# Performance work log

Measured on AMD Instinct MI355X. Metric: run time of the kernel, lower is better.

Reference implementation:

```python
import jax, jax.numpy as jnp
import numpy as np

H = 16          # num_heads
LN_EPS = 1e-5


def _layernorm(x, g, b):
    mu = jnp.mean(x, axis=-1, keepdims=True)
    var = jnp.mean(jnp.square(x - mu), axis=-1, keepdims=True)
    return (x - mu) * jax.lax.rsqrt(var + LN_EPS) * g + b


def setup_inputs() -> dict:
    key = jax.random.key(0)
    ks = jax.random.split(key, 4)
    B, T, D = 32, 1024, 1024
    s = 1.0 / np.sqrt(D)
    return {
        "x": jax.random.normal(ks[0], (B, T, D), dtype=jnp.float32),
        "ln_g": jnp.ones((D,), jnp.float32),
        "ln_b": jnp.zeros((D,), jnp.float32),
        "Wq": jax.random.normal(ks[1], (D, D), dtype=jnp.float32) * s,
        "bq": jnp.zeros((D,), jnp.float32),
        "Wk": jax.random.normal(ks[2], (D, D), dtype=jnp.float32) * s,
        "bk": jnp.zeros((D,), jnp.float32),
        "Wv": jax.random.normal(ks[3], (D, D), dtype=jnp.float32) * s,
        "bv": jnp.zeros((D,), jnp.float32),
    }


def reference(x, ln_g, ln_b, Wq, bq, Wk, bk, Wv, bv):
    B, T, D = x.shape
    d = D // H
    xn = _layernorm(x, ln_g, ln_b)                       # [B,T,D]
    # torch Linear: y = x @ W.T + b, W is [out, in]
    q = jnp.einsum('btd,ed->bte', xn, Wq) + bq
    k = jnp.einsum('btd,ed->bte', xn, Wk) + bk
    v = (jnp.einsum('btd,ed->bte', xn, Wv) + bv).reshape(B, T, H, d)
    q = jax.nn.softmax(q.reshape(B, T, H, d), axis=-1)   # softmax over head dim
    k = jax.nn.softmax(k.reshape(B, T, H, d), axis=1)    # softmax over sequence
    # linear attention: context [B,H,d,d], then project queries through it
    attn = jnp.einsum('bnhd,bnhl->bhdl', k, v)
    y = jnp.einsum('bnhd,bhdl->bnhl', q, attn).reshape(B, T, D)
    return x + y
```

## Files before the change

### kernel.cpp

```cpp
#include <hip/hip_runtime.h>
#include <stdint.h>

typedef __attribute__((ext_vector_type(4))) float  f32x4;
typedef __attribute__((ext_vector_type(8))) short  short8;
typedef __attribute__((ext_vector_type(4))) short  short4v;
typedef __attribute__((ext_vector_type(2))) unsigned int uint2v;

#define DEV __device__ __forceinline__

DEV float b2f(unsigned short u) { return __uint_as_float(((unsigned)u) << 16); }
DEV unsigned short f2b(float f) {
  unsigned u = __float_as_uint(f);
  return (unsigned short)((u + 0x7fffu + ((u >> 16) & 1u)) >> 16);
}

#define AS1C(p) ((const __attribute__((address_space(1))) void*)(uintptr_t)(p))
#define AS3(p)  ((__attribute__((address_space(3))) void*)(unsigned)(uintptr_t)(p))
DEV void gload16(const void* g, void* l) {
  __builtin_amdgcn_global_load_lds(AS1C(g), AS3(l), 16, 0, 0);
}

static constexpr int B_ = 32, T_ = 1024, D_ = 1024;
static constexpr int M_ = B_ * T_;
static constexpr int N3 = 3 * D_;

__global__ __launch_bounds__(256) void prep_kernel(
    const float* __restrict__ Wq, const float* __restrict__ Wk, const float* __restrict__ Wv,
    const float* __restrict__ bq, const float* __restrict__ bk, const float* __restrict__ bv,
    const float* __restrict__ x, const float* __restrict__ lng, const float* __restrict__ lnb,
    unsigned short* __restrict__ Wcat, float* __restrict__ bias,
    float* __restrict__ ksum, unsigned short* __restrict__ xn)
{
  int bid = blockIdx.x;
  int tid = threadIdx.x;
  if (bid < 3072) {
    int idx = bid * 256 + tid;
    int which = idx >> 18;
    int rem   = idx & 262143;
    const float* src = which == 0 ? Wq : (which == 1 ? Wk : Wv);
    f32x4 v = reinterpret_cast<const f32x4*>(src)[rem];
    uint2v p;
    p[0] = (unsigned)f2b(v[0]) | ((unsigned)f2b(v[1]) << 16);
    p[1] = (unsigned)f2b(v[2]) | ((unsigned)f2b(v[3]) << 16);
    reinterpret_cast<uint2v*>(Wcat)[idx] = p;
    if (idx < 3072) {
      const float* bsrc = idx < 1024 ? bq : (idx < 2048 ? bk : bv);
      bias[idx] = bsrc[idx & 1023];
    }
    if (idx < 32768) ksum[idx] = 0.f;
    return;
  }
  int row = bid - 3072;
  const f32x4 v = reinterpret_cast<const f32x4*>(x + (size_t)row * D_)[tid];
  float s  = v[0] + v[1] + v[2] + v[3];
  float s2 = v[0]*v[0] + v[1]*v[1] + v[2]*v[2] + v[3]*v[3];
  #pragma unroll
  for (int o = 32; o > 0; o >>= 1) { s += __shfl_down(s, o); s2 += __shfl_down(s2, o); }
  __shared__ float rs_[4], rs2_[4];
  int lane = tid & 63, wave = tid >> 6;
  if (lane == 0) { rs_[wave] = s; rs2_[wave] = s2; }
  __syncthreads();
  float S  = rs_[0] + rs_[1] + rs_[2] + rs_[3];
  float S2 = rs2_[0] + rs2_[1] + rs2_[2] + rs2_[3];
  float mu = S * (1.f / D_);
  float var = S2 * (1.f / D_) - mu * mu;
  float rstd = rsqrtf(var + 1e-5f);
  const f32x4 gg = reinterpret_cast<const f32x4*>(lng)[tid];
  const f32x4 bb = reinterpret_cast<const f32x4*>(lnb)[tid];
  float y0 = (v[0]-mu)*rstd*gg[0] + bb[0];
  float y1 = (v[1]-mu)*rstd*gg[1] + bb[1];
  float y2 = (v[2]-mu)*rstd*gg[2] + bb[2];
  float y3 = (v[3]-mu)*rstd*gg[3] + bb[3];
  uint2v p;
  p[0] = (unsigned)f2b(y0) | ((unsigned)f2b(y1) << 16);
  p[1] = (unsigned)f2b(y2) | ((unsigned)f2b(y3) << 16);
  reinterpret_cast<uint2v*>(xn + (size_t)row * D_)[tid] = p;
}

__global__ __launch_bounds__(512, 2) void gemm_qkv(
    const unsigned short* __restrict__ A,
    const unsigned short* __restrict__ Bm,
    const float* __restrict__ bias,
    unsigned short* __restrict__ C,
    float* __restrict__ ksum)
{
  __shared__ alignas(16) short lds[4 * 16384];
  const int tid = threadIdx.x;
  constexpr int nbn = N3 / 256;
  constexpr int nwg = (M_ / 256) * nbn;
  int wg = blockIdx.x;
  int swzb = (wg & 7) * (nwg >> 3) + (wg >> 3);
  int bm = swzb / nbn, bn = swzb % nbn;
  int arow = bm * 256, bcol = bn * 256;
  int lane = tid & 63, wave = tid >> 6;
  int wr = wave >> 2, wc = wave & 3;
  int g = lane >> 4, r = lane & 15;

  const unsigned short* Ab = A  + (size_t)arow * 1024;
  const unsigned short* Bb = Bm + (size_t)bcol * 1024;

  int rho = (wave << 4) | (lane >> 2);
  int pg  = (lane & 3) ^ ((rho >> 1) & 3);
  size_t gR0 = (size_t)rho * 1024 + pg * 8;
  size_t gR1 = (size_t)(rho + 128) * 1024 + pg * 8;
  int lofs = wave * 512;

  #define STAGE_A(t) { short* bb0 = lds + (((t) & 3) << 14); int k2 = (t) << 5; \
    gload16(Ab + k2 + gR0, (void*)(bb0 + lofs)); \
    gload16(Ab + k2 + gR1, (void*)(bb0 + 4096 + lofs)); }
  #define STAGE_B(t) { short* bb0 = lds + (((t) & 3) << 14); int k2 = (t) << 5; \
    gload16(Bb + k2 + gR0, (void*)(bb0 + 8192 + lofs)); \
    gload16(Bb + k2 + gR1, (void*)(bb0 + 12288 + lofs)); }

  f32x4 acc[8][4] = {};
  STAGE_A(0); STAGE_B(0);
  STAGE_A(1); STAGE_B(1);
  STAGE_A(2); STAGE_B(2);
  asm volatile("s_waitcnt vmcnt(8)" ::: "memory");
  __builtin_amdgcn_s_barrier();

  for (int t = 0; t < 32; ++t) {
    const short* bufA = lds + ((t & 3) << 14);
    const short* bufB = bufA + 8192;
    short8 a[8], bfr[4];
    #pragma unroll
    for (int mi = 0; mi < 8; ++mi) {
      int row = wr * 128 + mi * 16 + r;
      a[mi] = *(const short8*)(bufA + row * 32 + ((g ^ ((row >> 1) & 3)) << 3));
    }
    #pragma unroll
    for (int ni = 0; ni < 4; ++ni) {
      int row = wc * 64 + ni * 16 + r;
      bfr[ni] = *(const short8*)(bufB + row * 32 + ((g ^ ((row >> 1) & 3)) << 3));
    }
    if (t < 29) { STAGE_A(t + 3); STAGE_B(t + 3); }
    __builtin_amdgcn_s_setprio(1);
    #pragma unroll
    for (int mi = 0; mi < 8; ++mi)
      #pragma unroll
      for (int ni = 0; ni < 4; ++ni)
        acc[mi][ni] = __builtin_amdgcn_mfma_f32_16x16x32_bf16(a[mi], bfr[ni], acc[mi][ni], 0, 0, 0);
    __builtin_amdgcn_s_setprio(0);
    if (t < 29)       { asm volatile("s_waitcnt vmcnt(8)" ::: "memory"); }
    else if (t == 29) { asm volatile("s_waitcnt vmcnt(4)" ::: "memory"); }
    else if (t == 30) { asm volatile("s_waitcnt vmcnt(0)" ::: "memory"); }
    __builtin_amdgcn_s_barrier();
  }
  #undef STAGE_A
  #undef STAGE_B

  float bs[4];
  #pragma unroll
  for (int ni = 0; ni < 4; ++ni) bs[ni] = bias[bcol + wc * 64 + ni * 16 + r];
  bool isK = (bcol >= 1024 && bcol < 2048);
  if (isK) {
    float ks[4] = {0.f, 0.f, 0.f, 0.f};
    #pragma unroll
    for (int mi = 0; mi < 8; ++mi)
      #pragma unroll
      for (int j = 0; j < 4; ++j) {
        int rowl = wr * 128 + mi * 16 + 4 * g + j;
        size_t rb = (size_t)(arow + rowl) * N3 + bcol + wc * 64 + r;
        #pragma unroll
        for (int ni = 0; ni < 4; ++ni) {
          unsigned short cv = f2b(acc[mi][ni][j] + bs[ni]);
          C[rb + ni * 16] = cv;
          ks[ni] += __expf(b2f(cv));
        }
      }
    int b = arow >> 10;
    #pragma unroll
    for (int ni = 0; ni < 4; ++ni) {
      float s = ks[ni];
      s += __shfl_xor(s, 16);
      s += __shfl_xor(s, 32);
      if (g == 0)
        atomicAdd(&ksum[b * 1024 + (bcol - 1024) + wc * 64 + ni * 16 + r], s);
    }
  } else {
    #pragma unroll
    for (int mi = 0; mi < 8; ++mi)
      #pragma unroll
      for (int j = 0; j < 4; ++j) {
        int rowl = wr * 128 + mi * 16 + 4 * g + j;
        size_t rb = (size_t)(arow + rowl) * N3 + bcol + wc * 64 + r;
        #pragma unroll
        for (int ni = 0; ni < 4; ++ni)
          C[rb + ni * 16] = f2b(acc[mi][ni][j] + bs[ni]);
      }
  }
}

__global__ __launch_bounds__(256) void attn_kernel(
    const unsigned short* __restrict__ qkv, const float* __restrict__ ksum,
    unsigned short* __restrict__ attnP)
{
  int bid = blockIdx.x;
  int bh = bid >> 2, tq = bid & 3;
  int b = bh >> 4, h = bh & 15;
  int tid = threadIdx.x;
  int cgrp = tid & 7, trow = tid >> 3;
  int lane = tid & 63, wave = tid >> 6;
  int g = lane >> 4, r = lane & 15;
  __shared__ alignas(16) short lK[64 * 40];
  __shared__ alignas(16) short lV[64 * 40];
  const unsigned short* kb = qkv + ((size_t)(b * T_ + tq * 256)) * N3 + D_     + h * 64;
  const unsigned short* vb = qkv + ((size_t)(b * T_ + tq * 256)) * N3 + 2 * D_ + h * 64;
  float inv[8];
  const float* kp = ksum + b * 1024 + h * 64 + cgrp * 8;
  #pragma unroll
  for (int j = 0; j < 8; ++j) inv[j] = 1.f / kp[j];
  f32x4 acc[4] = {};
  short8 kv = *(const short8*)(kb + (size_t)trow * N3 + cgrp * 8);
  short8 vv = *(const short8*)(vb + (size_t)trow * N3 + cgrp * 8);
  for (int tc = 0; tc < 8; ++tc) {
    __syncthreads();
    #pragma unroll
    for (int j = 0; j < 8; ++j) {
      lK[(cgrp * 8 + j) * 40 + trow] =
          (short)f2b(__expf(b2f((unsigned short)kv[j])) * inv[j]);
      lV[(cgrp * 8 + j) * 40 + trow] = vv[j];
    }
    __syncthreads();
    if (tc < 7) {
      kv = *(const short8*)(kb + (size_t)((tc + 1) * 32 + trow) * N3 + cgrp * 8);
      vv = *(const short8*)(vb + (size_t)((tc + 1) * 32 + trow) * N3 + cgrp * 8);
    }
    short8 af = *(const short8*)(lK + (16 * wave + r) * 40 + 8 * g);
    #pragma unroll
    for (int ni = 0; ni < 4; ++ni) {
      short8 bf = *(const short8*)(lV + (16 * ni + r) * 40 + 8 * g);
      acc[ni] = __builtin_amdgcn_mfma_f32_16x16x32_bf16(af, bf, acc[ni], 0, 0, 0);
    }
  }
  unsigned short* op = attnP + (size_t)bid * 4096;
  #pragma unroll
  for (int ni = 0; ni < 4; ++ni)
    #pragma unroll
    for (int j = 0; j < 4; ++j) {
      int m = 16 * wave + 4 * g + j;
      int n = 16 * ni + r;
      op[(size_t)n * 64 + m] = f2b(acc[ni][j]);
    }
}

__global__ __launch_bounds__(256) void attn_reduce(
    const unsigned short* __restrict__ attnP, unsigned short* __restrict__ attnT)
{
  int bh = blockIdx.x;
  int tid = threadIdx.x;
  const unsigned short* p0 = attnP + ((size_t)bh << 2) * 4096;
  unsigned short* o = attnT + (size_t)bh * 4096;
  #pragma unroll
  for (int it = 0; it < 2; ++it) {
    int i = (it * 256 + tid) * 8;
    short8 s0 = *(const short8*)(p0 + i);
    short8 s1 = *(const short8*)(p0 + 4096 + i);
    short8 s2 = *(const short8*)(p0 + 8192 + i);
    short8 s3 = *(const short8*)(p0 + 12288 + i);
    short8 ov;
    #pragma unroll
    for (int j = 0; j < 8; ++j) {
      float s = b2f((unsigned short)s0[j]) + b2f((unsigned short)s1[j])
              + b2f((unsigned short)s2[j]) + b2f((unsigned short)s3[j]);
      ov[j] = (short)f2b(s);
    }
    *(short8*)(o + i) = ov;
  }
}

__global__ __launch_bounds__(256) void out_kernel(
    const unsigned short* __restrict__ qkv, const unsigned short* __restrict__ attnT,
    const float* __restrict__ x, float* __restrict__ out)
{
  int bid = blockIdx.x;
  int bh = bid >> 3, mt = bid & 7;
  int b = bh >> 4, h = bh & 15;
  int tid = threadIdx.x;
  int lane = tid & 63, wave = tid >> 6;
  int g = lane >> 4, r = lane & 15;
  __shared__ alignas(16) short lAT[64 * 72];
  __shared__ float lO[128][66];
  int rr = tid >> 4, c4 = (tid & 15) << 2;
  f32x4 xv[8];
  #pragma unroll
  for (int p = 0; p < 8; ++p) {
    int rowl = p * 16 + rr;
    size_t gi = ((size_t)(b * T_ + mt * 128 + rowl) << 10) + h * 64 + c4;
    xv[p] = *(const f32x4*)(x + gi);
  }
  const unsigned short* at = attnT + (size_t)bh * 4096;
  #pragma unroll
  for (int i = 0; i < 2; ++i) {
    int idx8 = (i * 256 + tid) * 8;
    int n = idx8 >> 6, kk0 = idx8 & 63;
    *(short8*)(lAT + n * 72 + kk0) = *(const short8*)(at + idx8);
  }
  __syncthreads();
  short8 bt[4][2];
  #pragma unroll
  for (int ni = 0; ni < 4; ++ni)
    #pragma unroll
    for (int kc = 0; kc < 2; ++kc)
      bt[ni][kc] = *(const short8*)(lAT + (16 * ni + r) * 72 + kc * 32 + 8 * g);
  int rowbase = mt * 128 + 32 * wave;
  const unsigned short* qb = qkv + (size_t)(b * T_ + rowbase) * N3 + h * 64;
  short8 aq[2][2];
  #pragma unroll
  for (int mi = 0; mi < 2; ++mi) {
    float qe[16];
    float s = 0.f;
    #pragma unroll
    for (int kc = 0; kc < 2; ++kc) {
      short8 qa = *(const short8*)(qb + (size_t)(16 * mi + r) * N3 + kc * 32 + 8 * g);
      #pragma unroll
      for (int j = 0; j < 8; ++j) {
        float e = __expf(b2f((unsigned short)qa[j]));
        qe[kc * 8 + j] = e;
        s += e;
      }
    }
    s += __shfl_xor(s, 16);
    s += __shfl_xor(s, 32);
    float inv = 1.f / s;
    #pragma unroll
    for (int kc = 0; kc < 2; ++kc) {
      short8 t8;
      #pragma unroll
      for (int j = 0; j < 8; ++j) t8[j] = (short)f2b(qe[kc * 8 + j] * inv);
      aq[mi][kc] = t8;
    }
  }
  f32x4 acc[2][4] = {};
  #pragma unroll
  for (int mi = 0; mi < 2; ++mi)
    #pragma unroll
    for (int kc = 0; kc < 2; ++kc)
      #pragma unroll
      for (int ni = 0; ni < 4; ++ni)
        acc[mi][ni] = __builtin_amdgcn_mfma_f32_16x16x32_bf16(aq[mi][kc], bt[ni][kc], acc[mi][ni], 0, 0, 0);
  #pragma unroll
  for (int mi = 0; mi < 2; ++mi)
    #pragma unroll
    for (int ni = 0; ni < 4; ++ni)
      #pragma unroll
      for (int j = 0; j < 4; ++j)
        lO[32 * wave + 16 * mi + 4 * g + j][16 * ni + r] = acc[mi][ni][j];
  __syncthreads();
  #pragma unroll
  for (int p = 0; p < 8; ++p) {
    int rowl = p * 16 + rr;
    size_t gi = ((size_t)(b * T_ + mt * 128 + rowl) << 10) + h * 64 + c4;
    f32x4 ov;
    ov[0] = xv[p][0] + lO[rowl][c4];
    ov[1] = xv[p][1] + lO[rowl][c4 + 1];
    ov[2] = xv[p][2] + lO[rowl][c4 + 2];
    ov[3] = xv[p][3] + lO[rowl][c4 + 3];
    *(f32x4*)(out + gi) = ov;
  }
}

extern "C" void kernel_launch(void* const* d_in, const int* in_sizes, int n_in,
                              void* d_out, int out_size, void* d_ws, size_t ws_size,
                              hipStream_t stream) {
  const float* x   = (const float*)d_in[0];
  const float* lng = (const float*)d_in[1];
  const float* lnb = (const float*)d_in[2];
  const float* Wq  = (const float*)d_in[3];
  const float* bq  = (const float*)d_in[4];
  const float* Wk  = (const float*)d_in[5];
  const float* bk  = (const float*)d_in[6];
  const float* Wv  = (const float*)d_in[7];
  const float* bv  = (const float*)d_in[8];
  float* out = (float*)d_out;
  char* ws = (char*)d_ws;
  unsigned short* Wcat  = (unsigned short*)(ws + 0);
  float*          bias  = (float*)         (ws + 6291456);
  unsigned short* xn    = (unsigned short*)(ws + 6303744);
  unsigned short* qkv   = (unsigned short*)(ws + 73412608);
  unsigned short* attnT = (unsigned short*)(ws + 274739200);
  unsigned short* attnP = (unsigned short*)xn;
  float* ksum = (float*)d_out;
  prep_kernel<<<3072 + M_, 256, 0, stream>>>(Wq, Wk, Wv, bq, bk, bv,
                                             x, lng, lnb, Wcat, bias, ksum, xn);
  gemm_qkv   <<<1536,  512, 0, stream>>>(xn, Wcat, bias, qkv, ksum);
  attn_kernel<<<2048,  256, 0, stream>>>(qkv, ksum, attnP);
  attn_reduce<<<512,   256, 0, stream>>>(attnP, attnT);
  out_kernel <<<4096,  256, 0, stream>>>(qkv, attnT, x, out);
}
```

Before: 374.9 us.

## Process head pairs per attn block and stage Q through LDS in out_kernel

attn_kernel now handles two adjacent heads per block, so each thread loads 16-byte K/V chunks spanning 128 contiguous columns and the grid halves to 1024 blocks. This gives wider coalesced row segments per global load. out_kernel now stages the 128x64 Q tile into LDS (aliased onto the output staging buffer) with coalesced row loads, instead of each lane doing strided global reads. It adds an extra barrier before the buffer is reused. The cost is more LDS per attn block and fewer blocks available for latency hiding.

```diff
diff --git a/kernel.cpp b/kernel.cpp
--- a/kernel.cpp
+++ b/kernel.cpp
@@ -196,52 +196,65 @@
     unsigned short* __restrict__ attnP)
 {
   int bid = blockIdx.x;
-  int bh = bid >> 2, tq = bid & 3;
-  int b = bh >> 4, h = bh & 15;
+  int b = bid >> 5, hp = (bid >> 2) & 7, tq = bid & 3;
   int tid = threadIdx.x;
-  int cgrp = tid & 7, trow = tid >> 3;
+  int cgrp = tid & 15, trow = tid >> 4;
   int lane = tid & 63, wave = tid >> 6;
   int g = lane >> 4, r = lane & 15;
-  __shared__ alignas(16) short lK[64 * 40];
-  __shared__ alignas(16) short lV[64 * 40];
-  const unsigned short* kb = qkv + ((size_t)(b * T_ + tq * 256)) * N3 + D_     + h * 64;
-  const unsigned short* vb = qkv + ((size_t)(b * T_ + tq * 256)) * N3 + 2 * D_ + h * 64;
+  __shared__ alignas(16) short lK[128 * 40];
+  __shared__ alignas(16) short lV[128 * 40];
+  const unsigned short* kb = qkv + ((size_t)(b * T_ + tq * 256)) * N3 + D_     + hp * 128;
+  const unsigned short* vb = qkv + ((size_t)(b * T_ + tq * 256)) * N3 + 2 * D_ + hp * 128;
   float inv[8];
-  const float* kp = ksum + b * 1024 + h * 64 + cgrp * 8;
+  const float* kp = ksum + b * 1024 + hp * 128 + cgrp * 8;
   #pragma unroll
   for (int j = 0; j < 8; ++j) inv[j] = 1.f / kp[j];
-  f32x4 acc[4] = {};
-  short8 kv = *(const short8*)(kb + (size_t)trow * N3 + cgrp * 8);
-  short8 vv = *(const short8*)(vb + (size_t)trow * N3 + cgrp * 8);
+  f32x4 acc[2][4] = {};
+  short8 kv0 = *(const short8*)(kb + (size_t)trow * N3 + cgrp * 8);
+  short8 kv1 = *(const short8*)(kb + (size_t)(16 + trow) * N3 + cgrp * 8);
+  short8 vv0 = *(const short8*)(vb + (size_t)trow * N3 + cgrp * 8);
+  short8 vv1 = *(const short8*)(vb + (size_t)(16 + trow) * N3 + cgrp * 8);
   for (int tc = 0; tc < 8; ++tc) {
     __syncthreads();
     #pragma unroll
     for (int j = 0; j < 8; ++j) {
-      lK[(cgrp * 8 + j) * 40 + trow] =
-          (short)f2b(__expf(b2f((unsigned short)kv[j])) * inv[j]);
-      lV[(cgrp * 8 + j) * 40 + trow] = vv[j];
+      int col = cgrp * 8 + j;
+      lK[col * 40 + trow]      = (short)f2b(__expf(b2f((unsigned short)kv0[j])) * inv[j]);
+      lK[col * 40 + 16 + trow] = (short)f2b(__expf(b2f((unsigned short)kv1[j])) * inv[j]);
+      lV[col * 40 + trow]      = vv0[j];
+      lV[col * 40 + 16 + trow] = vv1[j];
     }
     __syncthreads();
     if (tc < 7) {
-      kv = *(const short8*)(kb + (size_t)((tc + 1) * 32 + trow) * N3 + cgrp * 8);
-      vv = *(const short8*)(vb + (size_t)((tc + 1) * 32 + trow) * N3 + cgrp * 8);
-    }
-    short8 af = *(const short8*)(lK + (16 * wave + r) * 40 + 8 * g);
-    #pragma unroll
-    for (int ni = 0; ni < 4; ++ni) {
-      short8 bf = *(const short8*)(lV + (16 * ni + r) * 40 + 8 * g);
-      acc[ni] = __builtin_amdgcn_mfma_f32_16x16x32_bf16(af, bf, acc[ni], 0, 0, 0);
-    }
-  }
-  unsigned short* op = attnP + (size_t)bid * 4096;
-  #pragma unroll
-  for (int ni = 0; ni < 4; ++ni)
-    #pragma unroll
-    for (int j = 0; j < 4; ++j) {
-      int m = 16 * wave + 4 * g + j;
-      int n = 16 * ni + r;
-      op[(size_t)n * 64 + m] = f2b(acc[ni][j]);
-    }
+      int t0 = (tc + 1) * 32;
+      kv0 = *(const short8*)(kb + (size_t)(t0 + trow) * N3 + cgrp * 8);
+      kv1 = *(const short8*)(kb + (size_t)(t0 + 16 + trow) * N3 + cgrp * 8);
+      vv0 = *(const short8*)(vb + (size_t)(t0 + trow) * N3 + cgrp * 8);
+      vv1 = *(const short8*)(vb + (size_t)(t0 + 16 + trow) * N3 + cgrp * 8);
+    }
+    #pragma unroll
+    for (int hh = 0; hh < 2; ++hh) {
+      short8 af = *(const short8*)(lK + (hh * 64 + 16 * wave + r) * 40 + 8 * g);
+      #pragma unroll
+      for (int ni = 0; ni < 4; ++ni) {
+        short8 bf = *(const short8*)(lV + (hh * 64 + 16 * ni + r) * 40 + 8 * g);
+        acc[hh][ni] = __builtin_amdgcn_mfma_f32_16x16x32_bf16(af, bf, acc[hh][ni], 0, 0, 0);
+      }
+    }
+  }
+  #pragma unroll
+  for (int hh = 0; hh < 2; ++hh) {
+    int bh = b * 16 + hp * 2 + hh;
+    unsigned short* op = attnP + ((size_t)(bh * 4 + tq)) * 4096;
+    #pragma unroll
+    for (int ni = 0; ni < 4; ++ni)
+      #pragma unroll
+      for (int j = 0; j < 4; ++j) {
+        int m = 16 * wave + 4 * g + j;
+        int n = 16 * ni + r;
+        op[(size_t)n * 64 + m] = f2b(acc[hh][ni][j]);
+      }
+  }
 }
 
 __global__ __launch_bounds__(256) void attn_reduce(
@@ -280,7 +293,8 @@
   int lane = tid & 63, wave = tid >> 6;
   int g = lane >> 4, r = lane & 15;
   __shared__ alignas(16) short lAT[64 * 72];
-  __shared__ float lO[128][66];
+  __shared__ alignas(16) float lO[128][66];
+  short* lQ = reinterpret_cast<short*>(&lO[0][0]);
   int rr = tid >> 4, c4 = (tid & 15) << 2;
   f32x4 xv[8];
   #pragma unroll
@@ -296,6 +310,14 @@
     int n = idx8 >> 6, kk0 = idx8 & 63;
     *(short8*)(lAT + n * 72 + kk0) = *(const short8*)(at + idx8);
   }
+  const unsigned short* qbase = qkv + (size_t)(b * T_ + mt * 128) * N3 + h * 64;
+  #pragma unroll
+  for (int p = 0; p < 4; ++p) {
+    int idx = p * 256 + tid;
+    int qrow = idx >> 3, grp = idx & 7;
+    *(short8*)(lQ + qrow * 72 + grp * 8) =
+        *(const short8*)(qbase + (size_t)qrow * N3 + grp * 8);
+  }
   __syncthreads();
   short8 bt[4][2];
   #pragma unroll
@@ -303,16 +325,15 @@
     #pragma unroll
     for (int kc = 0; kc < 2; ++kc)
       bt[ni][kc] = *(const short8*)(lAT + (16 * ni + r) * 72 + kc * 32 + 8 * g);
-  int rowbase = mt * 128 + 32 * wave;
-  const unsigned short* qb = qkv + (size_t)(b * T_ + rowbase) * N3 + h * 64;
   short8 aq[2][2];
   #pragma unroll
   for (int mi = 0; mi < 2; ++mi) {
+    int qrow = 32 * wave + 16 * mi + r;
     float qe[16];
     float s = 0.f;
     #pragma unroll
     for (int kc = 0; kc < 2; ++kc) {
-      short8 qa = *(const short8*)(qb + (size_t)(16 * mi + r) * N3 + kc * 32 + 8 * g);
+      short8 qa = *(const short8*)(lQ + qrow * 72 + kc * 32 + 8 * g);
       #pragma unroll
       for (int j = 0; j < 8; ++j) {
         float e = __expf(b2f((unsigned short)qa[j]));
@@ -331,6 +352,7 @@
       aq[mi][kc] = t8;
     }
   }
+  __syncthreads();
   f32x4 acc[2][4] = {};
   #pragma unroll
   for (int mi = 0; mi < 2; ++mi)
@@ -384,7 +406,7 @@
   prep_kernel<<<3072 + M_, 256, 0, stream>>>(Wq, Wk, Wv, bq, bk, bv,
                                              x, lng, lnb, Wcat, bias, ksum, xn);
   gemm_qkv   <<<1536,  512, 0, stream>>>(xn, Wcat, bias, qkv, ksum);
-  attn_kernel<<<2048,  256, 0, stream>>>(qkv, ksum, attnP);
+  attn_kernel<<<1024,  256, 0, stream>>>(qkv, ksum, attnP);
   attn_reduce<<<512,   256, 0, stream>>>(attnP, attnT);
   out_kernel <<<4096,  256, 0, stream>>>(qkv, attnT, x, out);
 }
```

New measurement: 394.6 us. 5.3% more time.
